# Kernel tuning notes

Hardware: AMD Instinct MI355X
Metric: run time of the kernel (lower is better)

## Reference

```python
import jax, jax.numpy as jnp
import numpy as np

NUM_HEADS = 8
ALPHA = 0.01  # leaky_relu slope
MAX_SEQ = 64


def layer_norm(x, g, b, eps=1e-5):
    m = jnp.mean(x, axis=-1, keepdims=True)
    v = jnp.var(x, axis=-1, keepdims=True)
    return (x - m) * jax.lax.rsqrt(v + eps) * g + b


def ff(x, w1, b1, w2, b2):
    # Linear -> exact GELU -> Linear (torch nn.GELU default is erf-based)
    return jax.nn.gelu(x @ w1.T + b1, approximate=False) @ w2.T + b2


def mha(q, k, v, in_w, in_b, out_w, out_b, kpm):
    # torch nn.MultiheadAttention, batch_first=False. q:[Tq,E,d], k/v:[Tk,E,d], kpm:[E,Tk] True=pad
    d = q.shape[-1]
    H = NUM_HEADS
    dh = d // H
    qp = q @ in_w[:d].T + in_b[:d]
    kp = k @ in_w[d:2 * d].T + in_b[d:2 * d]
    vp = v @ in_w[2 * d:].T + in_b[2 * d:]
    Tq, E, _ = qp.shape
    Tk = kp.shape[0]
    qh = qp.reshape(Tq, E, H, dh) * (dh ** -0.5)
    kh = kp.reshape(Tk, E, H, dh)
    vh = vp.reshape(Tk, E, H, dh)
    scores = jnp.einsum('qehd,kehd->ehqk', qh, kh)  # [E,H,Tq,Tk]
    scores = jnp.where(kpm[:, None, None, :], jnp.float32(-1e9), scores)
    att = jax.nn.softmax(scores, axis=-1)
    out = jnp.einsum('ehqk,kehd->qehd', att, vh).reshape(Tq, E, d)
    return out @ out_w.T + out_b


def setup_inputs() -> dict:
    key = jax.random.key(0)
    ks = jax.random.split(key, 40)
    N, d, E, Seq, H = 50000, 64, 150000, 5, NUM_HEADS

    def xn(k, shape, scale):
        return jax.random.normal(k, shape, dtype=jnp.float32) * scale

    inp = {
        'features': xn(ks[0], (N, d), 1.0),
        'pos_emb': xn(ks[1], (MAX_SEQ, d), 0.02),
        'self_in_w': xn(ks[2], (3 * d, d), 0.1),
        'self_in_b': jnp.zeros((3 * d,), jnp.float32),
        'self_out_w': xn(ks[3], (d, d), 0.1),
        'self_out_b': jnp.zeros((d,), jnp.float32),
        'cross_in_w': xn(ks[4], (3 * d, d), 0.1),
        'cross_in_b': jnp.zeros((3 * d,), jnp.float32),
        'cross_out_w': xn(ks[5], (d, d), 0.1),
        'cross_out_b': jnp.zeros((d,), jnp.float32),
        'sa_ln1_g': jnp.ones((d,), jnp.float32), 'sa_ln1_b': jnp.zeros((d,), jnp.float32),
        'sa_ln2_g': jnp.ones((d,), jnp.float32), 'sa_ln2_b': jnp.zeros((d,), jnp.float32),
        'ca_ln1_g': jnp.ones((d,), jnp.float32), 'ca_ln1_b': jnp.zeros((d,), jnp.float32),
        'ca_ln2_g': jnp.ones((d,), jnp.float32), 'ca_ln2_b': jnp.zeros((d,), jnp.float32),
        'sa_ff_w1': xn(ks[6], (4 * d, d), 0.08), 'sa_ff_b1': jnp.zeros((4 * d,), jnp.float32),
        'sa_ff_w2': xn(ks[7], (d, 4 * d), 0.08), 'sa_ff_b2': jnp.zeros((d,), jnp.float32),
        'ca_ff_w1': xn(ks[8], (4 * d, d), 0.08), 'ca_ff_b1': jnp.zeros((4 * d,), jnp.float32),
        'ca_ff_w2': xn(ks[9], (d, 4 * d), 0.08), 'ca_ff_b2': jnp.zeros((d,), jnp.float32),
        'inst_w': xn(ks[10], (NUM_HEADS * d, d), 0.08),
        'attn_vec': xn(ks[11], (1, NUM_HEADS, d), 0.2),
        'edge_metapath_indices': jax.random.randint(ks[12], (E, Seq), 0, N, dtype=jnp.int64)
            if jax.config.jax_enable_x64 else jax.random.randint(ks[12], (E, Seq), 0, N).astype(jnp.int32),
        'dst': jax.random.randint(ks[13], (E,), 0, N).astype(jnp.int32),
    }
    inp['edge_metapath_indices'] = inp['edge_metapath_indices'].astype(jnp.int32)
    return inp


def reference(features, pos_emb, self_in_w, self_in_b, self_out_w, self_out_b,
              cross_in_w, cross_in_b, cross_out_w, cross_out_b,
              sa_ln1_g, sa_ln1_b, sa_ln2_g, sa_ln2_b,
              ca_ln1_g, ca_ln1_b, ca_ln2_g, ca_ln2_b,
              sa_ff_w1, sa_ff_b1, sa_ff_w2, sa_ff_b2,
              ca_ff_w1, ca_ff_b1, ca_ff_w2, ca_ff_b2,
              inst_w, attn_vec, edge_metapath_indices, dst):
    N, d = features.shape
    pad_id = N  # module pads one zero row; indices == pad_id are padding
    feats = jnp.concatenate([features, jnp.zeros((1, d), features.dtype)], axis=0)
    idx = edge_metapath_indices  # [E, Seq]
    E, Seq = idx.shape
    kpm = idx == pad_id  # [E, Seq] key padding mask

    edata = feats[idx]  # [E, Seq, d] gather (embedding)
    tokens = jnp.transpose(edata, (1, 0, 2))  # [Seq, E, d]
    pos_vec = pos_emb[:Seq][:, None, :]  # [Seq, 1, d]
    pos_vec = jnp.where(kpm.T[:, :, None], jnp.float32(0.0), pos_vec)
    tokens = tokens + pos_vec  # pos_drop is identity in eval

    # pre-LN self-attention block over the metapath sequence
    sa_in = layer_norm(tokens, sa_ln1_g, sa_ln1_b)
    tokens = tokens + mha(sa_in, sa_in, sa_in, self_in_w, self_in_b, self_out_w, self_out_b, kpm)
    sa_out = jnp.transpose(tokens, (1, 0, 2))  # [E, Seq, d]

    valid = (~kpm).astype(features.dtype)  # [E, Seq]
    denom = jnp.clip(valid.sum(axis=1, keepdims=True), 1.0, None)
    inst_emb = (sa_out * valid[:, :, None]).sum(axis=1) / denom  # masked mean pool
    inst_emb = inst_emb + ff(layer_norm(inst_emb, sa_ln2_g, sa_ln2_b), sa_ff_w1, sa_ff_b1, sa_ff_w2, sa_ff_b2)

    # cross-attention: last (target) node attends over the sequence
    lengths = (~kpm).sum(axis=1)
    last_pos = jnp.clip(lengths - 1, 0, None)
    last_ids = jnp.take_along_axis(idx, last_pos[:, None], axis=1)[:, 0]
    target_feat = feats[last_ids]
    q = layer_norm(target_feat, ca_ln1_g, ca_ln1_b)[None]  # [1, E, d]
    cross_out = mha(q, tokens, tokens, cross_in_w, cross_in_b, cross_out_w, cross_out_b, kpm)
    inst_emb = inst_emb + cross_out[0]
    inst_emb = inst_emb + ff(layer_norm(inst_emb, ca_ln2_g, ca_ln2_b), ca_ff_w1, ca_ff_b1, ca_ff_w2, ca_ff_b2)

    # heads projection, leaky-relu attention score, edge softmax, scatter-sum
    eft = (inst_emb @ inst_w.T).reshape(E, NUM_HEADS, d)  # [E, H, d]
    a = jnp.sum(eft * attn_vec, axis=-1)  # [E, H]
    a = jnp.where(a > 0, a, ALPHA * a)  # leaky_relu
    seg_max = jax.ops.segment_max(a, dst, num_segments=N)  # per-dst-node max
    a_exp = jnp.exp(a - seg_max[dst])
    seg_sum = jax.ops.segment_sum(a_exp, dst, num_segments=N)
    att = a_exp / seg_sum[dst]  # edge_softmax; attn_drop=0 -> identity
    ret = jax.ops.segment_sum(eft * att[:, :, None], dst, num_segments=N)  # [N, H, d]
    return ret
```

## Files before the change

kernel.cpp:

```cpp
#include <hip/hip_runtime.h>
#include <math.h>

#define D 64
#define LOG2E 1.44269504088896340736f
#define QSCALE (0.35355339059327373f * LOG2E)

typedef float f32x4 __attribute__((ext_vector_type(4)));
typedef float vf4 __attribute__((ext_vector_type(4)));
typedef short bf16x8 __attribute__((ext_vector_type(8)));
typedef unsigned short ushort_t;
typedef unsigned int uint2v __attribute__((ext_vector_type(2)));

#define MF(a, b, c) __builtin_amdgcn_mfma_f32_16x16x32_bf16(a, b, c, 0, 0, 0)

__device__ __forceinline__ float bcast(float x, int i) {
  return __int_as_float(__builtin_amdgcn_readlane(__float_as_int(x), i));
}

__device__ __forceinline__ float xs16(float x) {
#if __has_builtin(__builtin_amdgcn_permlane16_swap)
  uint2v a = __builtin_amdgcn_permlane16_swap(__float_as_uint(x), __float_as_uint(x), false, false);
  return __uint_as_float(a[0]) + __uint_as_float(a[1]);
#else
  return x + __shfl_xor(x, 16);
#endif
}
__device__ __forceinline__ float xs32(float x) {
#if __has_builtin(__builtin_amdgcn_permlane32_swap)
  uint2v a = __builtin_amdgcn_permlane32_swap(__float_as_uint(x), __float_as_uint(x), false, false);
  return __uint_as_float(a[0]) + __uint_as_float(a[1]);
#else
  return x + __shfl_xor(x, 32);
#endif
}
__device__ __forceinline__ float qsum(float x) {
  return xs32(xs16(x));
}

__device__ __forceinline__ ushort_t f2b(float f) {
  unsigned int u = __float_as_uint(f);
  unsigned int r = (u + 0x7FFFu + ((u >> 16) & 1u)) >> 16;
  return (ushort_t)r;
}
__device__ __forceinline__ unsigned int pkrtne(float lo, float hi) {
  unsigned int a = __float_as_uint(lo);
  unsigned int b = __float_as_uint(hi);
  a = a + 0x7FFFu + ((a >> 16) & 1u);
  b = b + 0x7FFFu + ((b >> 16) & 1u);
  return __builtin_amdgcn_perm(b, a, 0x07060302u);
}
__device__ __forceinline__ f32x4 ld4(const float* __restrict__ p) { return *(const f32x4*)p; }
__device__ __forceinline__ bf16x8 mkpair(const f32x4& ce, const f32x4& co) {
  union { bf16x8 v; unsigned int w[4]; } u;
  u.w[0] = pkrtne(ce[0], ce[1]);
  u.w[1] = pkrtne(ce[2], ce[3]);
  u.w[2] = pkrtne(co[0], co[1]);
  u.w[3] = pkrtne(co[2], co[3]);
  return u.v;
}
__device__ __forceinline__ f32x4 unpk(bf16x8 p, int half) {
  union { bf16x8 v; unsigned int w[4]; } u;
  u.v = p;
  unsigned int w0 = u.w[half * 2], w1 = u.w[half * 2 + 1];
  f32x4 r;
  r[0] = __uint_as_float(w0 << 16);
  r[1] = __uint_as_float(w0 & 0xFFFF0000u);
  r[2] = __uint_as_float(w1 << 16);
  r[3] = __uint_as_float(w1 & 0xFFFF0000u);
  return r;
}

__device__ __forceinline__ void lnT(const f32x4 (&x)[4], f32x4 (&y)[4],
                                    const float* __restrict__ g, const float* __restrict__ b,
                                    int quad) {
  float s1 = 0.f, s2 = 0.f;
#pragma unroll
  for (int ct = 0; ct < 4; ct++)
#pragma unroll
    for (int r = 0; r < 4; r++) { s1 += x[ct][r]; s2 += x[ct][r] * x[ct][r]; }
  s1 = qsum(s1);
  s2 = qsum(s2);
  float mean = s1 * 0.015625f;
  float var = s2 * 0.015625f - mean * mean;
  float rs = rsqrtf(var + 1e-5f);
#pragma unroll
  for (int ct = 0; ct < 4; ct++) {
    f32x4 gv = ld4(g + 16 * ct + 4 * quad);
    f32x4 bv = ld4(b + 16 * ct + 4 * quad);
#pragma unroll
    for (int r = 0; r < 4; r++) y[ct][r] = (x[ct][r] - mean) * rs * gv[r] + bv[r];
  }
}

__global__ void zero_kernel(float4* __restrict__ p, int n4) {
  int t = blockIdx.x * blockDim.x + threadIdx.x;
  if (t < n4) p[t] = make_float4(0.f, 0.f, 0.f, 0.f);
}

__global__ void prep_kernel(const float* __restrict__ si, const float* __restrict__ so,
                            const float* __restrict__ w1s, const float* __restrict__ w2s,
                            const float* __restrict__ ci, const float* __restrict__ co,
                            const float* __restrict__ w1c, const float* __restrict__ w2c,
                            const float* __restrict__ iw, const float* __restrict__ av,
                            float* __restrict__ ws) {
  int t = blockIdx.x * blockDim.x + threadIdx.x;
  ushort_t* bw = (ushort_t*)(ws + 33280);
  if (t < 98304) {
    const float* src;
    int base, cs;
    int l = t;
    if      (l < 12288) { src = si;  base = 0;     cs = 6; }
    else if (l < 16384) { src = so;  base = 12288; cs = 6; l -= 12288; }
    else if (l < 32768) { src = w1s; base = 16384; cs = 6; l -= 16384; }
    else if (l < 49152) { src = w2s; base = 32768; cs = 8; l -= 32768; }
    else if (l < 61440) { src = ci;  base = 49152; cs = 6; l -= 49152; }
    else if (l < 65536) { src = co;  base = 61440; cs = 6; l -= 61440; }
    else if (l < 81920) { src = w1c; base = 65536; cs = 6; l -= 65536; }
    else                { src = w2c; base = 81920; cs = 8; l -= 81920; }
    int c = l >> cs, k = l & ((1 << cs) - 1);
    int T = (1 << cs) >> 5;
    int ct = c >> 4, m = c & 15, tt = k >> 5, rem = k & 31;
    int quad = (rem >> 2) & 3;
    int j = (((rem >> 4) & 1) << 2) | (rem & 3);
    bw[base + (size_t)((ct * T + tt) * 64 + quad * 16 + m) * 8 + j] = f2b(src[l]);
  } else if (t < 131072) {
    int l = t - 98304;
    int c = l >> 6, k = l & 63;
    ws[(k >> 2) * 2048 + c * 4 + (k & 3)] = iw[l];
  } else if (t < 131584) {
    int l = t - 131072;
    int h = l >> 6, k = l & 63;
    float acc = 0.f;
    for (int c = 0; c < 64; c++) acc += av[h * 64 + c] * iw[(h * 64 + c) * 64 + k];
    ws[32768 + h * 64 + k] = acc;
  }
}

#define SC1(KARR, QF, CT, KS, P)                                                        \
  { f32x4 kv_ = unpk(KARR[KS][(CT) >> 1], (CT) & 1);                                    \
    float sp_ = QF[CT][0] * kv_[0] + QF[CT][1] * kv_[1] + QF[CT][2] * kv_[2] +          \
                QF[CT][3] * kv_[3];                                                     \
    sp_ = xs16(sp_);                                                                    \
    P = ((vb >> (KS)) & 1) ? sp_ : -1e30f; }

#define PV1(VARR, CT, KS, P, ACC)                                                       \
  { f32x4 vv_ = unpk(VARR[KS][(CT) >> 1], (CT) & 1);                                    \
    _Pragma("unroll") for (int r = 0; r < 4; r++) ACC[r] = fmaf(P, vv_[r], ACC[r]); }

#define ATT_CT(KARR, VARR, QF, CT, OD)                                                  \
  {                                                                                     \
    float p0, p1, p2, p3, p4;                                                           \
    SC1(KARR, QF, CT, 0, p0); SC1(KARR, QF, CT, 1, p1); SC1(KARR, QF, CT, 2, p2);       \
    SC1(KARR, QF, CT, 3, p3); SC1(KARR, QF, CT, 4, p4);                                 \
    float mx_ = fmaxf(fmaxf(fmaxf(p0, p1), fmaxf(p2, p3)), p4);                         \
    p0 = exp2f(p0 - mx_); p1 = exp2f(p1 - mx_); p2 = exp2f(p2 - mx_);                   \
    p3 = exp2f(p3 - mx_); p4 = exp2f(p4 - mx_);                                         \
    float ri_ = 1.0f / (p0 + p1 + p2 + p3 + p4);                                        \
    p0 *= ri_; p1 *= ri_; p2 *= ri_; p3 *= ri_; p4 *= ri_;                              \
    OD = (f32x4){0.f, 0.f, 0.f, 0.f};                                                   \
    PV1(VARR, CT, 0, p0, OD); PV1(VARR, CT, 1, p1, OD); PV1(VARR, CT, 2, p2, OD);       \
    PV1(VARR, CT, 3, p3, OD); PV1(VARR, CT, 4, p4, OD);                                 \
  }

#define KV_STAGE(S)                                                                     \
  {                                                                                     \
    f32x4 t[4], y[4];                                                                   \
    const bool vd = (vb >> (S)) & 1;                                                    \
    const float* fp = features + (size_t)min(ids[S], N - 1) * 64;                       \
    _Pragma("unroll")                                                                   \
    for (int ct = 0; ct < 4; ct++) {                                                    \
      f32x4 f = ld4(fp + 16 * ct + 4 * quad);                                           \
      f32x4 pv = ld4(pos_emb + (S) * 64 + 16 * ct + 4 * quad);                          \
      _Pragma("unroll")                                                                 \
      for (int r = 0; r < 4; r++) t[ct][r] = vd ? (f[r] + pv[r]) : 0.f;                 \
    }                                                                                   \
    lnT(t, y, sa_ln1_g, sa_ln1_b, quad);                                                \
    bf16x8 xl0 = mkpair(y[0], y[1]), xl1 = mkpair(y[2], y[3]);                          \
    f32x4 kt[4], vt[4];                                                                 \
    _Pragma("unroll")                                                                   \
    for (int ct = 0; ct < 4; ct++) {                                                    \
      f32x4 c = {0.f, 0.f, 0.f, 0.f};                                                   \
      c = MF(WSI[((4 + ct) * 2 + 0) * 64 + lane], xl0, c);                              \
      c = MF(WSI[((4 + ct) * 2 + 1) * 64 + lane], xl1, c);                              \
      f32x4 bb = ld4(self_in_b + 64 + 16 * ct + 4 * quad);                              \
      _Pragma("unroll")                                                                 \
      for (int r = 0; r < 4; r++) kt[ct][r] = c[r] + bb[r];                             \
      f32x4 c2 = {0.f, 0.f, 0.f, 0.f};                                                  \
      c2 = MF(WSI[((8 + ct) * 2 + 0) * 64 + lane], xl0, c2);                            \
      c2 = MF(WSI[((8 + ct) * 2 + 1) * 64 + lane], xl1, c2);                            \
      f32x4 bb2 = ld4(self_in_b + 128 + 16 * ct + 4 * quad);                            \
      _Pragma("unroll")                                                                 \
      for (int r = 0; r < 4; r++) vt[ct][r] = c2[r] + bb2[r];                           \
    }                                                                                   \
    Kp[S][0] = mkpair(kt[0], kt[1]); Kp[S][1] = mkpair(kt[2], kt[3]);                   \
    Vp[S][0] = mkpair(vt[0], vt[1]); Vp[S][1] = mkpair(vt[2], vt[3]);                   \
  }

#define Q_STAGE(S)                                                                      \
  {                                                                                     \
    const bool vd = (vb >> (S)) & 1;                                                    \
    const float* fp = features + (size_t)min(ids[S], N - 1) * 64;                       \
    f32x4 t[4], y[4];                                                                   \
    _Pragma("unroll")                                                                   \
    for (int ct = 0; ct < 4; ct++) {                                                    \
      f32x4 f = ld4(fp + 16 * ct + 4 * quad);                                           \
      f32x4 pv = ld4(pos_emb + (S) * 64 + 16 * ct + 4 * quad);                          \
      _Pragma("unroll")                                                                 \
      for (int r = 0; r < 4; r++) t[ct][r] = vd ? (f[r] + pv[r]) : 0.f;                 \
    }                                                                                   \
    lnT(t, y, sa_ln1_g, sa_ln1_b, quad);                                                \
    bf16x8 xl0 = mkpair(y[0], y[1]), xl1 = mkpair(y[2], y[3]);                          \
    f32x4 qf[4];                                                                        \
    _Pragma("unroll")                                                                   \
    for (int ct = 0; ct < 4; ct++) {                                                    \
      f32x4 c = {0.f, 0.f, 0.f, 0.f};                                                   \
      c = MF(WSI[(ct * 2 + 0) * 64 + lane], xl0, c);                                    \
      c = MF(WSI[(ct * 2 + 1) * 64 + lane], xl1, c);                                    \
      f32x4 bb = ld4(self_in_b + 16 * ct + 4 * quad);                                   \
      _Pragma("unroll")                                                                 \
      for (int r = 0; r < 4; r++) qf[ct][r] = (c[r] + bb[r]) * QSCALE;                  \
    }                                                                                   \
    f32x4 oa0, oa1, oa2, oa3;                                                           \
    ATT_CT(Kp, Vp, qf, 0, oa0); ATT_CT(Kp, Vp, qf, 1, oa1);                             \
    ATT_CT(Kp, Vp, qf, 2, oa2); ATT_CT(Kp, Vp, qf, 3, oa3);                             \
    bf16x8 op0 = mkpair(oa0, oa1), op1 = mkpair(oa2, oa3);                              \
    f32x4 tpc[4];                                                                       \
    _Pragma("unroll")                                                                   \
    for (int ct = 0; ct < 4; ct++) {                                                    \
      f32x4 c = {0.f, 0.f, 0.f, 0.f};                                                   \
      c = MF(WSO[(ct * 2 + 0) * 64 + lane], op0, c);                                    \
      c = MF(WSO[(ct * 2 + 1) * 64 + lane], op1, c);                                    \
      f32x4 bb = ld4(self_out_b + 16 * ct + 4 * quad);                                  \
      _Pragma("unroll")                                                                 \
      for (int r = 0; r < 4; r++) {                                                     \
        float tp_ = c[r] + bb[r] + t[ct][r];                                            \
        tpc[ct][r] = tp_;                                                               \
        pool[ct][r] += vd ? tp_ : 0.f;                                                  \
      }                                                                                 \
    }                                                                                   \
    TP[S][0] = mkpair(tpc[0], tpc[1]); TP[S][1] = mkpair(tpc[2], tpc[3]);               \
  }

#define CKV_STAGE(S)                                                                    \
  {                                                                                     \
    f32x4 kt[4], vt[4];                                                                 \
    _Pragma("unroll")                                                                   \
    for (int ct = 0; ct < 4; ct++) {                                                    \
      f32x4 c = {0.f, 0.f, 0.f, 0.f};                                                   \
      c = MF(WCI[((4 + ct) * 2 + 0) * 64 + lane], TP[S][0], c);                         \
      c = MF(WCI[((4 + ct) * 2 + 1) * 64 + lane], TP[S][1], c);                         \
      f32x4 bb = ld4(cross_in_b + 64 + 16 * ct + 4 * quad);                             \
      _Pragma("unroll")                                                                 \
      for (int r = 0; r < 4; r++) kt[ct][r] = c[r] + bb[r];                             \
      f32x4 c2 = {0.f, 0.f, 0.f, 0.f};                                                  \
      c2 = MF(WCI[((8 + ct) * 2 + 0) * 64 + lane], TP[S][0], c2);                       \
      c2 = MF(WCI[((8 + ct) * 2 + 1) * 64 + lane], TP[S][1], c2);                       \
      f32x4 bb2 = ld4(cross_in_b + 128 + 16 * ct + 4 * quad);                           \
      _Pragma("unroll")                                                                 \
      for (int r = 0; r < 4; r++) vt[ct][r] = c2[r] + bb2[r];                           \
    }                                                                                   \
    Kc[S][0] = mkpair(kt[0], kt[1]); Kc[S][1] = mkpair(kt[2], kt[3]);                   \
    Vc[S][0] = mkpair(vt[0], vt[1]); Vc[S][1] = mkpair(vt[2], vt[3]);                   \
  }

#define FF_H2(CT, HD)                                                                   \
  { f32x4 c = {0.f, 0.f, 0.f, 0.f};                                                     \
    c = MF(W1[((CT) * 2 + 0) * 64 + lane], x0, c);                                      \
    c = MF(W1[((CT) * 2 + 1) * 64 + lane], x1, c);                                      \
    f32x4 bb = ld4(b1 + 16 * (CT) + 4 * quad);                                          \
    _Pragma("unroll")                                                                   \
    for (int r = 0; r < 4; r++) {                                                       \
      float v = c[r] + bb[r];                                                           \
      HD[r] = 0.5f * v * (1.0f + erff(v * 0.70710678118654752440f));                    \
    } }

#define FF_O(CT)                                                                        \
  { f32x4 c = {0.f, 0.f, 0.f, 0.f};                                                     \
    c = MF(W2[((CT) * 8 + 0) * 64 + lane], Hp0, c);                                     \
    c = MF(W2[((CT) * 8 + 1) * 64 + lane], Hp1, c);                                     \
    c = MF(W2[((CT) * 8 + 2) * 64 + lane], Hp2, c);                                     \
    c = MF(W2[((CT) * 8 + 3) * 64 + lane], Hp3, c);                                     \
    c = MF(W2[((CT) * 8 + 4) * 64 + lane], Hp4, c);                                     \
    c = MF(W2[((CT) * 8 + 5) * 64 + lane], Hp5, c);                                     \
    c = MF(W2[((CT) * 8 + 6) * 64 + lane], Hp6, c);                                     \
    c = MF(W2[((CT) * 8 + 7) * 64 + lane], Hp7, c);                                     \
    f32x4 bb = ld4(b2 + 16 * (CT) + 4 * quad);                                          \
    _Pragma("unroll")                                                                   \
    for (int r = 0; r < 4; r++) inst[CT][r] += c[r] + bb[r]; }

__device__ __forceinline__ void ffnT(f32x4 (&inst)[4],
                                     const float* __restrict__ g, const float* __restrict__ b,
                                     const bf16x8* __restrict__ W1, const bf16x8* __restrict__ W2,
                                     const float* __restrict__ b1, const float* __restrict__ b2,
                                     int lane, int quad) {
  f32x4 y[4];
  lnT(inst, y, g, b, quad);
  bf16x8 x0 = mkpair(y[0], y[1]), x1 = mkpair(y[2], y[3]);
  f32x4 ha, hb;
  FF_H2(0, ha);  FF_H2(1, hb);  bf16x8 Hp0 = mkpair(ha, hb);
  FF_H2(2, ha);  FF_H2(3, hb);  bf16x8 Hp1 = mkpair(ha, hb);
  FF_H2(4, ha);  FF_H2(5, hb);  bf16x8 Hp2 = mkpair(ha, hb);
  FF_H2(6, ha);  FF_H2(7, hb);  bf16x8 Hp3 = mkpair(ha, hb);
  FF_H2(8, ha);  FF_H2(9, hb);  bf16x8 Hp4 = mkpair(ha, hb);
  FF_H2(10, ha); FF_H2(11, hb); bf16x8 Hp5 = mkpair(ha, hb);
  FF_H2(12, ha); FF_H2(13, hb); bf16x8 Hp6 = mkpair(ha, hb);
  FF_H2(14, ha); FF_H2(15, hb); bf16x8 Hp7 = mkpair(ha, hb);
  FF_O(0); FF_O(1); FF_O(2); FF_O(3);
}

#define ASC(H)                                                                          \
  { float sp = 0.f;                                                                     \
    _Pragma("unroll")                                                                   \
    for (int ct = 0; ct < 4; ct++) {                                                    \
      f32x4 uu = ld4(uvec + (H) * 64 + 16 * ct + 4 * quad);                             \
      _Pragma("unroll")                                                                 \
      for (int r = 0; r < 4; r++) sp = fmaf(inst[ct][r], uu[r], sp);                    \
    }                                                                                   \
    sp = qsum(sp);                                                                      \
    a##H = sp > 0.f ? sp : 0.01f * sp; }

__global__ __launch_bounds__(64, 1)
void edge_kernel(const float* __restrict__ features, const float* __restrict__ pos_emb,
                 const float* __restrict__ self_in_b, const float* __restrict__ self_out_b,
                 const float* __restrict__ cross_in_b, const float* __restrict__ cross_out_b,
                 const float* __restrict__ sa_ln1_g, const float* __restrict__ sa_ln1_b,
                 const float* __restrict__ sa_ln2_g, const float* __restrict__ sa_ln2_b,
                 const float* __restrict__ ca_ln1_g, const float* __restrict__ ca_ln1_b,
                 const float* __restrict__ ca_ln2_g, const float* __restrict__ ca_ln2_b,
                 const float* __restrict__ sa_ff_b1, const float* __restrict__ sa_ff_b2,
                 const float* __restrict__ ca_ff_b1, const float* __restrict__ ca_ff_b2,
                 const int* __restrict__ midx, const int* __restrict__ dstv,
                 const float* __restrict__ ws,
                 float* __restrict__ inst_out, float* __restrict__ a_out, int E, int N) {
  const int lane = threadIdx.x;
  const int quad = lane >> 4, lo = lane & 15;
  const int e0 = blockIdx.x * 16;
  __shared__ float xp[16 * 68];

  const ushort_t* bw = (const ushort_t*)(ws + 33280);
  const bf16x8* WSI = (const bf16x8*)(bw);
  const bf16x8* WSO = (const bf16x8*)(bw + 12288);
  const bf16x8* W1S = (const bf16x8*)(bw + 16384);
  const bf16x8* W2S = (const bf16x8*)(bw + 32768);
  const bf16x8* WCI = (const bf16x8*)(bw + 49152);
  const bf16x8* WCO = (const bf16x8*)(bw + 61440);
  const bf16x8* W1C = (const bf16x8*)(bw + 65536);
  const bf16x8* W2C = (const bf16x8*)(bw + 81920);
  const float* uvec = ws + 32768;

  const bool ge = (e0 + lo) < E;
  const int eIdx = min(e0 + lo, E - 1);
  int ids[5];
  ids[0] = midx[eIdx * 5 + 0];
  ids[1] = midx[eIdx * 5 + 1];
  ids[2] = midx[eIdx * 5 + 2];
  ids[3] = midx[eIdx * 5 + 3];
  ids[4] = midx[eIdx * 5 + 4];
  int vb = 0;
  if (ids[0] != N && ge) vb |= 1;
  if (ids[1] != N && ge) vb |= 2;
  if (ids[2] != N && ge) vb |= 4;
  if (ids[3] != N && ge) vb |= 8;
  if (ids[4] != N && ge) vb |= 16;
  const int nv = __popc(vb);
  const int lp = max(nv - 1, 0);
  int lid = ids[0];
  lid = (lp == 1) ? ids[1] : lid;
  lid = (lp == 2) ? ids[2] : lid;
  lid = (lp == 3) ? ids[3] : lid;
  lid = (lp == 4) ? ids[4] : lid;

  bf16x8 Kp[5][2], Vp[5][2];
  KV_STAGE(0); KV_STAGE(1); KV_STAGE(2); KV_STAGE(3); KV_STAGE(4);

  f32x4 pool[4];
#pragma unroll
  for (int ct = 0; ct < 4; ct++) pool[ct] = (f32x4){0.f, 0.f, 0.f, 0.f};
  bf16x8 TP[5][2];
  Q_STAGE(0); Q_STAGE(1); Q_STAGE(2); Q_STAGE(3); Q_STAGE(4);

  f32x4 inst[4];
  {
    float rn = 1.0f / (float)max(nv, 1);
#pragma unroll
    for (int ct = 0; ct < 4; ct++)
#pragma unroll
      for (int r = 0; r < 4; r++) inst[ct][r] = pool[ct][r] * rn;
  }

  ffnT(inst, sa_ln2_g, sa_ln2_b, W1S, W2S, sa_ff_b1, sa_ff_b2, lane, quad);

  {
    f32x4 tf[4], xq[4];
    const bool vdl = lid != N;
    const float* fp = features + (size_t)min(lid, N - 1) * 64;
#pragma unroll
    for (int ct = 0; ct < 4; ct++) {
      f32x4 f = ld4(fp + 16 * ct + 4 * quad);
#pragma unroll
      for (int r = 0; r < 4; r++) tf[ct][r] = vdl ? f[r] : 0.f;
    }
    lnT(tf, xq, ca_ln1_g, ca_ln1_b, quad);
    bf16x8 xq0 = mkpair(xq[0], xq[1]), xq1 = mkpair(xq[2], xq[3]);
    f32x4 qcf[4];
#pragma unroll
    for (int ct = 0; ct < 4; ct++) {
      f32x4 c = {0.f, 0.f, 0.f, 0.f};
      c = MF(WCI[(ct * 2 + 0) * 64 + lane], xq0, c);
      c = MF(WCI[(ct * 2 + 1) * 64 + lane], xq1, c);
      f32x4 bb = ld4(cross_in_b + 16 * ct + 4 * quad);
#pragma unroll
      for (int r = 0; r < 4; r++) qcf[ct][r] = (c[r] + bb[r]) * QSCALE;
    }
    bf16x8 Kc[5][2], Vc[5][2];
    CKV_STAGE(0); CKV_STAGE(1); CKV_STAGE(2); CKV_STAGE(3); CKV_STAGE(4);
    f32x4 cc0, cc1, cc2, cc3;
    ATT_CT(Kc, Vc, qcf, 0, cc0); ATT_CT(Kc, Vc, qcf, 1, cc1);
    ATT_CT(Kc, Vc, qcf, 2, cc2); ATT_CT(Kc, Vc, qcf, 3, cc3);
    bf16x8 cp0 = mkpair(cc0, cc1), cp1 = mkpair(cc2, cc3);
#pragma unroll
    for (int ct = 0; ct < 4; ct++) {
      f32x4 c = {0.f, 0.f, 0.f, 0.f};
      c = MF(WCO[(ct * 2 + 0) * 64 + lane], cp0, c);
      c = MF(WCO[(ct * 2 + 1) * 64 + lane], cp1, c);
      f32x4 bb = ld4(cross_out_b + 16 * ct + 4 * quad);
#pragma unroll
      for (int r = 0; r < 4; r++) inst[ct][r] += c[r] + bb[r];
    }
  }

  ffnT(inst, ca_ln2_g, ca_ln2_b, W1C, W2C, ca_ff_b1, ca_ff_b2, lane, quad);

  float a0, a1, a2, a3, a4, a5, a6, a7;
  ASC(0); ASC(1); ASC(2); ASC(3); ASC(4); ASC(5); ASC(6); ASC(7);
  if (ge && quad < 2) {
    f32x4 st = (quad == 0) ? (f32x4){a0, a1, a2, a3} : (f32x4){a4, a5, a6, a7};
    *(f32x4*)(a_out + (size_t)(e0 + lo) * 8 + 4 * quad) = st;
  }

#pragma unroll
  for (int ct = 0; ct < 4; ct++)
    *(f32x4*)(&xp[lo * 68 + 16 * ct + 4 * quad]) = inst[ct];
  __syncthreads();
  {
    int er = lane >> 2, cb = (lane & 3) * 16;
    if (e0 + er < E) {
#pragma unroll
      for (int u = 0; u < 4; u++) {
        f32x4 v = *(const f32x4*)(&xp[er * 68 + cb + 4 * u]);
        *(f32x4*)(inst_out + (size_t)(e0 + er) * 64 + cb + 4 * u) = v;
      }
    }
  }
}

__global__ void csr_count_kernel(const int* __restrict__ dstv, unsigned int* __restrict__ cnt,
                                 int E) {
  int e = blockIdx.x * blockDim.x + threadIdx.x;
  if (e < E) atomicAdd(&cnt[dstv[e]], 1u);
}

__global__ void scan1_kernel(unsigned int* __restrict__ off, unsigned int* __restrict__ bsum,
                             int N) {
  __shared__ unsigned int sd[256];
  int t = threadIdx.x, n = blockIdx.x * 256 + t;
  unsigned int v = (n < N) ? off[n] : 0u;
  sd[t] = v;
  __syncthreads();
  for (int o = 1; o < 256; o <<= 1) {
    unsigned int x = (t >= o) ? sd[t - o] : 0u;
    __syncthreads();
    sd[t] += x;
    __syncthreads();
  }
  if (n < N) off[n] = sd[t] - v;
  if (t == 255) bsum[blockIdx.x] = sd[255];
}

__global__ void scan2_kernel(unsigned int* __restrict__ bsum, int nb) {
  __shared__ unsigned int sd[1024];
  int t = threadIdx.x;
  unsigned int v = (t < nb) ? bsum[t] : 0u;
  sd[t] = v;
  __syncthreads();
  for (int o = 1; o < 1024; o <<= 1) {
    unsigned int x = (t >= o) ? sd[t - o] : 0u;
    __syncthreads();
    sd[t] += x;
    __syncthreads();
  }
  if (t < nb) bsum[t] = sd[t] - v;
}

__global__ void scan3_kernel(unsigned int* __restrict__ off, unsigned int* __restrict__ cur,
                             const unsigned int* __restrict__ bsum, int N, int E) {
  int n = blockIdx.x * 256 + threadIdx.x;
  if (n < N) {
    unsigned int o = off[n] + bsum[blockIdx.x];
    off[n] = o;
    cur[n] = o;
  }
  if (n == 0) off[N] = (unsigned int)E;
}

__global__ void csr_fill_kernel(const int* __restrict__ dstv, unsigned int* __restrict__ cur,
                                unsigned int* __restrict__ elist, int E) {
  int e = blockIdx.x * blockDim.x + threadIdx.x;
  if (e < E) {
    unsigned int p = atomicAdd(&cur[dstv[e]], 1u);
    elist[p] = (unsigned int)e;
  }
}

__global__ __launch_bounds__(256)
void att_kernel(const unsigned int* __restrict__ off, const unsigned int* __restrict__ elist,
                float* __restrict__ a, float* __restrict__ sinv, int N) {
  int n = blockIdx.x * blockDim.x + threadIdx.x;
  if (n >= N) return;
  const unsigned int s0 = off[n], s1 = off[n + 1];
  f32x4 m0 = {-3.0e38f, -3.0e38f, -3.0e38f, -3.0e38f}, m1 = m0;
  for (unsigned int i = s0; i < s1; i++) {
    const float* ap = a + (size_t)elist[i] * 8;
    f32x4 x0 = ld4(ap), x1 = ld4(ap + 4);
#pragma unroll
    for (int r = 0; r < 4; r++) { m0[r] = fmaxf(m0[r], x0[r]); m1[r] = fmaxf(m1[r], x1[r]); }
  }
  f32x4 t0 = {0.f, 0.f, 0.f, 0.f}, t1 = t0;
  for (unsigned int i = s0; i < s1; i++) {
    float* ap = a + (size_t)elist[i] * 8;
    f32x4 x0 = ld4(ap), x1 = ld4(ap + 4);
    f32x4 w0, w1;
#pragma unroll
    for (int r = 0; r < 4; r++) {
      w0[r] = __expf(x0[r] - m0[r]);
      w1[r] = __expf(x1[r] - m1[r]);
      t0[r] += w0[r];
      t1[r] += w1[r];
    }
    *(f32x4*)ap = w0;
    *(f32x4*)(ap + 4) = w1;
  }
  f32x4 r0, r1;
#pragma unroll
  for (int r = 0; r < 4; r++) {
    r0[r] = (t0[r] > 0.f) ? 1.0f / t0[r] : 0.f;
    r1[r] = (t1[r] > 0.f) ? 1.0f / t1[r] : 0.f;
  }
  *(f32x4*)(sinv + (size_t)n * 8) = r0;
  *(f32x4*)(sinv + (size_t)n * 8 + 4) = r1;
}

__global__ __launch_bounds__(256)
void gather_kernel(const float* __restrict__ T_iw, const unsigned int* __restrict__ off,
                   const unsigned int* __restrict__ elist, const float* __restrict__ a,
                   const float* __restrict__ sinv, const float* __restrict__ inst_emb,
                   float* __restrict__ out, int N) {
  const int lane = threadIdx.x & 63;
  const int widx = threadIdx.x >> 6;
  const int h = blockIdx.y;
  const vf4* P = (const vf4*)T_iw;
  vf4 wr[16];
#pragma unroll
  for (int k = 0; k < 16; k++) wr[k] = P[k * 512 + h * 64 + lane];
  const int stride = gridDim.x * 4;
  for (int n = blockIdx.x * 4 + widx; n < N; n += stride) {
    const unsigned int s0 = off[n], s1 = off[n + 1];
    float z = 0.f;
    for (unsigned int i = s0; i < s1; i++) {
      unsigned int e = elist[i];
      z = fmaf(a[(size_t)e * 8 + h], inst_emb[(size_t)e * 64 + lane], z);
    }
    z *= sinv[(size_t)n * 8 + h];
    float o = 0.f;
#pragma unroll
    for (int k = 0; k < 16; k++) {
#pragma unroll
      for (int u = 0; u < 4; u++) o = fmaf(bcast(z, k * 4 + u), wr[k][u], o);
    }
    out[(size_t)n * 512 + h * 64 + lane] = o;
  }
}

extern "C" void kernel_launch(void* const* d_in, const int* in_sizes, int n_in,
                              void* d_out, int out_size, void* d_ws, size_t ws_size,
                              hipStream_t stream) {
  const float* features   = (const float*)d_in[0];
  const float* pos_emb    = (const float*)d_in[1];
  const float* self_in_w  = (const float*)d_in[2];
  const float* self_in_b  = (const float*)d_in[3];
  const float* self_out_w = (const float*)d_in[4];
  const float* self_out_b = (const float*)d_in[5];
  const float* cross_in_w = (const float*)d_in[6];
  const float* cross_in_b = (const float*)d_in[7];
  const float* cross_out_w= (const float*)d_in[8];
  const float* cross_out_b= (const float*)d_in[9];
  const float* sa_ln1_g = (const float*)d_in[10];
  const float* sa_ln1_b = (const float*)d_in[11];
  const float* sa_ln2_g = (const float*)d_in[12];
  const float* sa_ln2_b = (const float*)d_in[13];
  const float* ca_ln1_g = (const float*)d_in[14];
  const float* ca_ln1_b = (const float*)d_in[15];
  const float* ca_ln2_g = (const float*)d_in[16];
  const float* ca_ln2_b = (const float*)d_in[17];
  const float* sa_ff_w1 = (const float*)d_in[18];
  const float* sa_ff_b1 = (const float*)d_in[19];
  const float* sa_ff_w2 = (const float*)d_in[20];
  const float* sa_ff_b2 = (const float*)d_in[21];
  const float* ca_ff_w1 = (const float*)d_in[22];
  const float* ca_ff_b1 = (const float*)d_in[23];
  const float* ca_ff_w2 = (const float*)d_in[24];
  const float* ca_ff_b2 = (const float*)d_in[25];
  const float* inst_w   = (const float*)d_in[26];
  const float* attn_vec = (const float*)d_in[27];
  const int* midx = (const int*)d_in[28];
  const int* dstv = (const int*)d_in[29];

  const int N = in_sizes[0] / 64;
  const int E = in_sizes[29];

  float* wsf = (float*)d_ws;
  float* inst_emb = wsf + 131072;
  float* a_arr = inst_emb + (size_t)E * 64;
  unsigned int* off = (unsigned int*)(a_arr + (size_t)E * 8);
  unsigned int* cur = off + (size_t)(N + 1);
  unsigned int* bsum = cur + (size_t)N;
  unsigned int* elist = bsum + 1024;
  float* sinv = (float*)(elist + (size_t)E);

  const int nb1 = (N + 255) / 256;

  {
    int n4 = (N + 1 + 3) / 4;
    zero_kernel<<<(n4 + 255) / 256, 256, 0, stream>>>((float4*)off, n4);
  }

  prep_kernel<<<(131584 + 255) / 256, 256, 0, stream>>>(
      self_in_w, self_out_w, sa_ff_w1, sa_ff_w2, cross_in_w, cross_out_w, ca_ff_w1, ca_ff_w2,
      inst_w, attn_vec, wsf);

  csr_count_kernel<<<(E + 255) / 256, 256, 0, stream>>>(dstv, off, E);
  scan1_kernel<<<nb1, 256, 0, stream>>>(off, bsum, N);
  scan2_kernel<<<1, 1024, 0, stream>>>(bsum, nb1);
  scan3_kernel<<<nb1, 256, 0, stream>>>(off, cur, bsum, N, E);
  csr_fill_kernel<<<(E + 255) / 256, 256, 0, stream>>>(dstv, cur, elist, E);

  int nblk = (E + 15) / 16;
  edge_kernel<<<nblk, 64, 0, stream>>>(
      features, pos_emb, self_in_b, self_out_b, cross_in_b, cross_out_b, sa_ln1_g, sa_ln1_b,
      sa_ln2_g, sa_ln2_b, ca_ln1_g, ca_ln1_b, ca_ln2_g, ca_ln2_b, sa_ff_b1, sa_ff_b2, ca_ff_b1,
      ca_ff_b2, midx, dstv, wsf, inst_emb, a_arr, E, N);

  att_kernel<<<nb1, 256, 0, stream>>>(off, elist, a_arr, sinv, N);

  dim3 ggrid(256, 8);
  gather_kernel<<<ggrid, 256, 0, stream>>>(wsf, off, elist, a_arr, sinv, inst_emb,
                                           (float*)d_out, N);
}
```

Measured before the change: 915.0 us.

## Spill TP stage buffers to LDS, raise edge occupancy, merge scan and zero launches

The per-stage bf16 TP fragments of edge_kernel move from registers into a shared LDS buffer that is aliased with the xp staging area, and launch bounds rise to two waves per EU so more waves can hide latency. The separate zero kernel is folded into prep_kernel, and the three-kernel CSR scan becomes one single-block 1024-thread scan with a running carry. Together these cut register pressure and launch count, at the cost of extra LDS traffic, a new barrier, and a serial single-block scan over N.

```diff
diff --git a/kernel.cpp b/kernel.cpp
--- a/kernel.cpp
+++ b/kernel.cpp
@@ -92,17 +92,12 @@
   }
 }
 
-__global__ void zero_kernel(float4* __restrict__ p, int n4) {
-  int t = blockIdx.x * blockDim.x + threadIdx.x;
-  if (t < n4) p[t] = make_float4(0.f, 0.f, 0.f, 0.f);
-}
-
 __global__ void prep_kernel(const float* __restrict__ si, const float* __restrict__ so,
                             const float* __restrict__ w1s, const float* __restrict__ w2s,
                             const float* __restrict__ ci, const float* __restrict__ co,
                             const float* __restrict__ w1c, const float* __restrict__ w2c,
                             const float* __restrict__ iw, const float* __restrict__ av,
-                            float* __restrict__ ws) {
+                            float* __restrict__ ws, unsigned int* __restrict__ zp, int zn) {
   int t = blockIdx.x * blockDim.x + threadIdx.x;
   ushort_t* bw = (ushort_t*)(ws + 33280);
   if (t < 98304) {
@@ -133,6 +128,8 @@
     float acc = 0.f;
     for (int c = 0; c < 64; c++) acc += av[h * 64 + c] * iw[(h * 64 + c) * 64 + k];
     ws[32768 + h * 64 + k] = acc;
+  } else if (t - 131584 < zn) {
+    zp[t - 131584] = 0u;
   }
 }
 
@@ -238,23 +235,26 @@
         pool[ct][r] += vd ? tp_ : 0.f;                                                  \
       }                                                                                 \
     }                                                                                   \
-    TP[S][0] = mkpair(tpc[0], tpc[1]); TP[S][1] = mkpair(tpc[2], tpc[3]);               \
+    tpS[((S) * 2 + 0) * 64 + lane] = mkpair(tpc[0], tpc[1]);                            \
+    tpS[((S) * 2 + 1) * 64 + lane] = mkpair(tpc[2], tpc[3]);                            \
   }
 
 #define CKV_STAGE(S)                                                                    \
   {                                                                                     \
+    bf16x8 tq0 = tpS[((S) * 2 + 0) * 64 + lane];                                        \
+    bf16x8 tq1 = tpS[((S) * 2 + 1) * 64 + lane];                                        \
     f32x4 kt[4], vt[4];                                                                 \
     _Pragma("unroll")                                                                   \
     for (int ct = 0; ct < 4; ct++) {                                                    \
       f32x4 c = {0.f, 0.f, 0.f, 0.f};                                                   \
-      c = MF(WCI[((4 + ct) * 2 + 0) * 64 + lane], TP[S][0], c);                         \
-      c = MF(WCI[((4 + ct) * 2 + 1) * 64 + lane], TP[S][1], c);                         \
+      c = MF(WCI[((4 + ct) * 2 + 0) * 64 + lane], tq0, c);                              \
+      c = MF(WCI[((4 + ct) * 2 + 1) * 64 + lane], tq1, c);                              \
       f32x4 bb = ld4(cross_in_b + 64 + 16 * ct + 4 * quad);                             \
       _Pragma("unroll")                                                                 \
       for (int r = 0; r < 4; r++) kt[ct][r] = c[r] + bb[r];                             \
       f32x4 c2 = {0.f, 0.f, 0.f, 0.f};                                                  \
-      c2 = MF(WCI[((8 + ct) * 2 + 0) * 64 + lane], TP[S][0], c2);                       \
-      c2 = MF(WCI[((8 + ct) * 2 + 1) * 64 + lane], TP[S][1], c2);                       \
+      c2 = MF(WCI[((8 + ct) * 2 + 0) * 64 + lane], tq0, c2);                            \
+      c2 = MF(WCI[((8 + ct) * 2 + 1) * 64 + lane], tq1, c2);                            \
       f32x4 bb2 = ld4(cross_in_b + 128 + 16 * ct + 4 * quad);                           \
       _Pragma("unroll")                                                                 \
       for (int r = 0; r < 4; r++) vt[ct][r] = c2[r] + bb2[r];                           \
@@ -319,7 +319,7 @@
     sp = qsum(sp);                                                                      \
     a##H = sp > 0.f ? sp : 0.01f * sp; }
 
-__global__ __launch_bounds__(64, 1)
+__global__ __launch_bounds__(64, 2)
 void edge_kernel(const float* __restrict__ features, const float* __restrict__ pos_emb,
                  const float* __restrict__ self_in_b, const float* __restrict__ self_out_b,
                  const float* __restrict__ cross_in_b, const float* __restrict__ cross_out_b,
@@ -335,7 +335,9 @@
   const int lane = threadIdx.x;
   const int quad = lane >> 4, lo = lane & 15;
   const int e0 = blockIdx.x * 16;
-  __shared__ float xp[16 * 68];
+  __shared__ __align__(16) ushort_t smem[5120];
+  bf16x8* tpS = (bf16x8*)smem;
+  float* xp = (float*)smem;
 
   const ushort_t* bw = (const ushort_t*)(ws + 33280);
   const bf16x8* WSI = (const bf16x8*)(bw);
@@ -376,7 +378,6 @@
   f32x4 pool[4];
 #pragma unroll
   for (int ct = 0; ct < 4; ct++) pool[ct] = (f32x4){0.f, 0.f, 0.f, 0.f};
-  bf16x8 TP[5][2];
   Q_STAGE(0); Q_STAGE(1); Q_STAGE(2); Q_STAGE(3); Q_STAGE(4);
 
   f32x4 inst[4];
@@ -438,6 +439,7 @@
     *(f32x4*)(a_out + (size_t)(e0 + lo) * 8 + 4 * quad) = st;
   }
 
+  __syncthreads();
 #pragma unroll
   for (int ct = 0; ct < 4; ct++)
     *(f32x4*)(&xp[lo * 68 + 16 * ct + 4 * quad]) = inst[ct];
@@ -460,47 +462,36 @@
   if (e < E) atomicAdd(&cnt[dstv[e]], 1u);
 }
 
-__global__ void scan1_kernel(unsigned int* __restrict__ off, unsigned int* __restrict__ bsum,
-                             int N) {
-  __shared__ unsigned int sd[256];
-  int t = threadIdx.x, n = blockIdx.x * 256 + t;
-  unsigned int v = (n < N) ? off[n] : 0u;
-  sd[t] = v;
+__global__ __launch_bounds__(1024)
+void csr_scan_kernel(unsigned int* __restrict__ off, unsigned int* __restrict__ cur,
+                     int N, int E) {
+  __shared__ unsigned int sd[1024];
+  __shared__ unsigned int carry;
+  const int t = threadIdx.x;
+  if (t == 0) carry = 0u;
   __syncthreads();
-  for (int o = 1; o < 256; o <<= 1) {
-    unsigned int x = (t >= o) ? sd[t - o] : 0u;
+  for (int base = 0; base < N; base += 1024) {
+    int n = base + t;
+    unsigned int v = (n < N) ? off[n] : 0u;
+    sd[t] = v;
     __syncthreads();
-    sd[t] += x;
+    for (int o = 1; o < 1024; o <<= 1) {
+      unsigned int x = (t >= o) ? sd[t - o] : 0u;
+      __syncthreads();
+      sd[t] += x;
+      __syncthreads();
+    }
+    unsigned int c = carry;
+    if (n < N) {
+      unsigned int o_ = c + sd[t] - v;
+      off[n] = o_;
+      cur[n] = o_;
+    }
     __syncthreads();
-  }
-  if (n < N) off[n] = sd[t] - v;
-  if (t == 255) bsum[blockIdx.x] = sd[255];
-}
-
-__global__ void scan2_kernel(unsigned int* __restrict__ bsum, int nb) {
-  __shared__ unsigned int sd[1024];
-  int t = threadIdx.x;
-  unsigned int v = (t < nb) ? bsum[t] : 0u;
-  sd[t] = v;
-  __syncthreads();
-  for (int o = 1; o < 1024; o <<= 1) {
-    unsigned int x = (t >= o) ? sd[t - o] : 0u;
+    if (t == 1023) carry = c + sd[1023];
     __syncthreads();
-    sd[t] += x;
-    __syncthreads();
-  }
-  if (t < nb) bsum[t] = sd[t] - v;
-}
-
-__global__ void scan3_kernel(unsigned int* __restrict__ off, unsigned int* __restrict__ cur,
-                             const unsigned int* __restrict__ bsum, int N, int E) {
-  int n = blockIdx.x * 256 + threadIdx.x;
-  if (n < N) {
-    unsigned int o = off[n] + bsum[blockIdx.x];
-    off[n] = o;
-    cur[n] = o;
-  }
-  if (n == 0) off[N] = (unsigned int)E;
+  }
+  if (t == 0) off[N] = (unsigned int)E;
 }
 
 __global__ void csr_fill_kernel(const int* __restrict__ dstv, unsigned int* __restrict__ cur,
@@ -623,25 +614,16 @@
   float* a_arr = inst_emb + (size_t)E * 64;
   unsigned int* off = (unsigned int*)(a_arr + (size_t)E * 8);
   unsigned int* cur = off + (size_t)(N + 1);
-  unsigned int* bsum = cur + (size_t)N;
-  unsigned int* elist = bsum + 1024;
+  unsigned int* elist = cur + (size_t)N;
   float* sinv = (float*)(elist + (size_t)E);
 
-  const int nb1 = (N + 255) / 256;
-
-  {
-    int n4 = (N + 1 + 3) / 4;
-    zero_kernel<<<(n4 + 255) / 256, 256, 0, stream>>>((float4*)off, n4);
-  }
-
-  prep_kernel<<<(131584 + 255) / 256, 256, 0, stream>>>(
+  int zn = N + 1;
+  prep_kernel<<<(131584 + zn + 255) / 256, 256, 0, stream>>>(
       self_in_w, self_out_w, sa_ff_w1, sa_ff_w2, cross_in_w, cross_out_w, ca_ff_w1, ca_ff_w2,
-      inst_w, attn_vec, wsf);
+      inst_w, attn_vec, wsf, off, zn);
 
   csr_count_kernel<<<(E + 255) / 256, 256, 0, stream>>>(dstv, off, E);
-  scan1_kernel<<<nb1, 256, 0, stream>>>(off, bsum, N);
-  scan2_kernel<<<1, 1024, 0, stream>>>(bsum, nb1);
-  scan3_kernel<<<nb1, 256, 0, stream>>>(off, cur, bsum, N, E);
+  csr_scan_kernel<<<1, 1024, 0, stream>>>(off, cur, N, E);
   csr_fill_kernel<<<(E + 255) / 256, 256, 0, stream>>>(dstv, cur, elist, E);
 
   int nblk = (E + 15) / 16;
@@ -650,7 +632,7 @@
       sa_ln2_g, sa_ln2_b, ca_ln1_g, ca_ln1_b, ca_ln2_g, ca_ln2_b, sa_ff_b1, sa_ff_b2, ca_ff_b1,
       ca_ff_b2, midx, dstv, wsf, inst_emb, a_arr, E, N);
 
-  att_kernel<<<nb1, 256, 0, stream>>>(off, elist, a_arr, sinv, N);
+  att_kernel<<<(N + 255) / 256, 256, 0, stream>>>(off, elist, a_arr, sinv, N);
 
   dim3 ggrid(256, 8);
   gather_kernel<<<ggrid, 256, 0, stream>>>(wsf, off, elist, a_arr, sinv, inst_emb,
```

Measured after the change: 1.045 ms. 1.14x slower.
